# Optimization experiments

Hardware: AMD Instinct MI355X
Metric: run time of the kernel (lower is better)

Reference implementation:

```python
import jax, jax.numpy as jnp
import numpy as np

T, H, W = 4, 16, 16
S = T * H * W          # 1024 flattened sequence length
C = 576                # embd_dim
NH = 8                 # n_head
DK = C // NH           # 72 per-head dim
L = 4                  # n_layer
B = 4                  # batch
PD = C // 3            # 192 per-axis pos-embed dim


def setup_inputs() -> dict:
    key = jax.random.key(0)
    ks = jax.random.split(key, 10)
    s = 1.0 / np.sqrt(C)
    return {
        "x": jax.random.normal(ks[0], (B, T, H, W, C), jnp.float32),
        "pos0": jax.random.normal(ks[1], (T, PD), jnp.float32) * 0.01,
        "pos1": jax.random.normal(ks[2], (H, PD), jnp.float32) * 0.01,
        "pos2": jax.random.normal(ks[3], (W, PD), jnp.float32) * 0.01,
        "ln1_g": jnp.ones((L, C), jnp.float32),
        "ln1_b": jnp.zeros((L, C), jnp.float32),
        "wq": jax.random.normal(ks[4], (L, C, C), jnp.float32) * s,
        "wk": jax.random.normal(ks[5], (L, C, C), jnp.float32) * s,
        "wv": jax.random.normal(ks[6], (L, C, C), jnp.float32) * s,
        "wo": jax.random.normal(ks[7], (L, C, C), jnp.float32) * (s / np.sqrt(L)),
        "wo_b": jnp.zeros((L, C), jnp.float32),
        "ln2_g": jnp.ones((L, C), jnp.float32),
        "ln2_b": jnp.zeros((L, C), jnp.float32),
        "w1": jax.random.normal(ks[8], (L, C, 4 * C), jnp.float32) * s,
        "b1": jnp.zeros((L, 4 * C), jnp.float32),
        "w2": jax.random.normal(ks[9], (L, 4 * C, C), jnp.float32) * (s / 2.0),
        "b2": jnp.zeros((L, C), jnp.float32),
    }


def _layernorm(x, g, b):
    # Faithful to the source: float32 math, and (1e-5 + rsqrt(var)) multiplier
    # (note: source adds eps to rsqrt, not to var -- replicated exactly).
    xf = x.astype(jnp.float32)
    mu = xf.mean(-1, keepdims=True)
    var = jnp.mean(jnp.square(xf - mu), -1, keepdims=True)
    y = (xf - mu) * (1e-5 + jax.lax.rsqrt(var)) * g + b
    return y.astype(x.dtype)


def _stack(x, pos0, pos1, pos2, ln1_g, ln1_b, wq, wk, wv, wo, wo_b,
           ln2_g, ln2_b, w1, b1, w2, b2):
    b = x.shape[0]
    xf = x.reshape(b, S, C)
    # right_shift (decode_step=None): shift flattened tokens right by one
    xf = jnp.pad(xf[:, :-1], ((0, 0), (1, 0), (0, 0)))
    # broadcast positional embedding, concat along channel
    pos = jnp.concatenate([
        jnp.broadcast_to(pos0[:, None, None, :], (T, H, W, PD)),
        jnp.broadcast_to(pos1[None, :, None, :], (T, H, W, PD)),
        jnp.broadcast_to(pos2[None, None, :, :], (T, H, W, PD)),
    ], axis=-1).reshape(S, C)
    xf = xf + pos

    causal = jnp.tril(jnp.ones((S, S), bool))
    scale = 1.0 / np.sqrt(DK)
    neg_inf = jnp.float32(-jnp.inf)

    for l in range(L):  # fixed small layer loop
        # --- causal full self-attention ---
        h = _layernorm(xf, ln1_g[l], ln1_b[l])
        q = (h @ wq[l]).reshape(b, S, NH, DK).transpose(0, 2, 1, 3)
        k = (h @ wk[l]).reshape(b, S, NH, DK).transpose(0, 2, 1, 3)
        v = (h @ wv[l]).reshape(b, S, NH, DK).transpose(0, 2, 1, 3)
        att = jnp.einsum('bhqd,bhkd->bhqk', q, k) * scale
        att = jnp.where(causal, att, neg_inf)
        att = jax.nn.softmax(att, axis=-1)
        a = jnp.einsum('bhqk,bhkd->bhqd', att, v)
        a = a.transpose(0, 2, 1, 3).reshape(b, S, C)
        xf = xf + a @ wo[l] + wo_b[l]
        # --- FFN with GeLU2: sigmoid(1.702*x)*x ---
        h = _layernorm(xf, ln2_g[l], ln2_b[l])
        h = h @ w1[l] + b1[l]
        h = jax.nn.sigmoid(1.702 * h) * h
        xf = xf + h @ w2[l] + b2[l]
    return xf.reshape(b, T, H, W, C)


def reference(x, pos0, pos1, pos2, ln1_g, ln1_b, wq, wk, wv, wo, wo_b,
              ln2_g, ln2_b, w1, b1, w2, b2):
    return _stack(x, pos0, pos1, pos2, ln1_g, ln1_b, wq, wk, wv, wo, wo_b,
                  ln2_g, ln2_b, w1, b1, w2, b2)
```

## Files before the change

### kernel.cpp

```cpp
#include <hip/hip_runtime.h>
#include <hip/hip_bf16.h>

typedef __hip_bfloat16 bf16;
using bf16x8 = __attribute__((ext_vector_type(8))) short;
using f32x4  = __attribute__((ext_vector_type(4))) float;

#define S_LEN 1024
#define CDIM  576
#define NHEAD 8
#define DKH   72
#define BATCH 4
#define MROWS 4096
#define FFDIM 2304
#define QKVN  1728

__device__ __forceinline__ void gload16(const void* g, void* l) {
  __builtin_amdgcn_global_load_lds(
      (const __attribute__((address_space(1))) unsigned int*)g,
      (__attribute__((address_space(3))) unsigned int*)l, 16, 0, 0);
}

template <int N> __device__ __forceinline__ void wait_vmcnt() {
  if constexpr (N == 0)      asm volatile("s_waitcnt vmcnt(0)" ::: "memory");
  else if constexpr (N == 2) asm volatile("s_waitcnt vmcnt(2)" ::: "memory");
  else if constexpr (N == 3) asm volatile("s_waitcnt vmcnt(3)" ::: "memory");
  else if constexpr (N == 4) asm volatile("s_waitcnt vmcnt(4)" ::: "memory");
  else if constexpr (N == 6) asm volatile("s_waitcnt vmcnt(6)" ::: "memory");
}

__device__ __forceinline__ short f2bf_bits(float x) {
  unsigned int u = __float_as_uint(x);
  u += 0x7fffu + ((u >> 16) & 1u);
  return (short)(u >> 16);
}

__device__ __forceinline__ void transpose_body(
    float (*tile)[33], const float* in, bf16* out, int K, int N,
    size_t in_ls, size_t out_ls, int bx, int by, int z) {
  const float* inl = in + (size_t)z * in_ls;
  bf16* outl = out + (size_t)z * out_ls;
  int n0 = bx * 32, k0 = by * 32;
  int tx = threadIdx.x & 31, ty = threadIdx.x >> 5;
#pragma unroll
  for (int i = 0; i < 32; i += 8)
    tile[ty + i][tx] = inl[(size_t)(k0 + ty + i) * N + (n0 + tx)];
  __syncthreads();
#pragma unroll
  for (int i = 0; i < 32; i += 8)
    outl[(size_t)(n0 + ty + i) * K + (k0 + tx)] = __float2bfloat16(tile[tx][ty + i]);
}

__global__ __launch_bounds__(256) void prologue(
    const float* __restrict__ wq, const float* __restrict__ wk,
    const float* __restrict__ wv, const float* __restrict__ wo,
    const float* __restrict__ w1, const float* __restrict__ w2,
    bf16* __restrict__ wqkvT, bf16* __restrict__ woT,
    bf16* __restrict__ w1T, bf16* __restrict__ w2T,
    const float* __restrict__ x, const float* __restrict__ p0,
    const float* __restrict__ p1, const float* __restrict__ p2,
    float* __restrict__ xf) {
  __shared__ float tile[32][33];
  const size_t ils  = (size_t)CDIM * CDIM;
  const size_t ils2 = (size_t)CDIM * FFDIM;
  const size_t qkv_ls = (size_t)QKVN * CDIM;
  int r = blockIdx.x;
  if (r < 5184) {
    int which = r / 1296, rr = r % 1296;
    int z = rr / 324, rem = rr % 324;
    int bx = rem % 18, by = rem / 18;
    const float* in; bf16* out; size_t ols;
    if (which == 0)      { in = wq; out = wqkvT;                       ols = qkv_ls; }
    else if (which == 1) { in = wk; out = wqkvT + (size_t)CDIM * CDIM; ols = qkv_ls; }
    else if (which == 2) { in = wv; out = wqkvT + (size_t)2 * CDIM * CDIM; ols = qkv_ls; }
    else                 { in = wo; out = woT;                         ols = ils; }
    transpose_body(tile, in, out, CDIM, CDIM, ils, ols, bx, by, z);
  } else if (r < 10368) {
    int rr = r - 5184;
    int z = rr / 1296, rem = rr % 1296;
    int bx = rem % 72, by = rem / 72;
    transpose_body(tile, w1, w1T, CDIM, FFDIM, ils2, ils2, bx, by, z);
  } else if (r < 15552) {
    int rr = r - 10368;
    int z = rr / 1296, rem = rr % 1296;
    int bx = rem % 18, by = rem / 18;
    transpose_body(tile, w2, w2T, FFDIM, CDIM, ils2, ils2, bx, by, z);
  } else {
    int idx = (r - 15552) * 256 + threadIdx.x;
    int c4 = idx % 144;
    int s  = (idx / 144) & (S_LEN - 1);
    int b  = idx / (144 * S_LEN);
    int c  = c4 * 4;
    int t = s >> 8, hh = (s >> 4) & 15, w = s & 15;
    float4 pv;
    if (c < 192)       pv = *(const float4*)&p0[t  * 192 + c];
    else if (c < 384)  pv = *(const float4*)&p1[hh * 192 + c - 192];
    else               pv = *(const float4*)&p2[w  * 192 + c - 384];
    float4 xv = make_float4(0.f, 0.f, 0.f, 0.f);
    if (s > 0) xv = *(const float4*)&x[((size_t)b * S_LEN + s - 1) * CDIM + c];
    float4 rr4 = make_float4(xv.x + pv.x, xv.y + pv.y, xv.z + pv.z, xv.w + pv.w);
    *(float4*)&xf[((size_t)b * S_LEN + s) * CDIM + c] = rr4;
  }
}

__global__ __launch_bounds__(256) void ln_kernel(
    const float* __restrict__ x, const float* __restrict__ g,
    const float* __restrict__ b, bf16* __restrict__ out) {
  int row  = blockIdx.x * 4 + (threadIdx.x >> 6);
  int lane = threadIdx.x & 63;
  const float* xr = x + (size_t)row * CDIM;
  float vals[9];
  float sum = 0.f;
#pragma unroll
  for (int i = 0; i < 9; i++) { vals[i] = xr[lane + 64 * i]; sum += vals[i]; }
#pragma unroll
  for (int o = 1; o < 64; o <<= 1) sum += __shfl_xor(sum, o);
  float mu = sum * (1.f / CDIM);
  float vs = 0.f;
#pragma unroll
  for (int i = 0; i < 9; i++) { float d = vals[i] - mu; vs += d * d; }
#pragma unroll
  for (int o = 1; o < 64; o <<= 1) vs += __shfl_xor(vs, o);
  float mult = 1e-5f + rsqrtf(vs * (1.f / CDIM));
  bf16* orow = out + (size_t)row * CDIM;
#pragma unroll
  for (int i = 0; i < 9; i++) {
    int c = lane + 64 * i;
    orow[c] = __float2bfloat16((vals[i] - mu) * mult * g[c] + b[c]);
  }
}

template <int BM, int BN, bool BIAS, bool RES, int ACT, bool OUTBF>
__global__ __launch_bounds__(256) void gemm3(
    const bf16* __restrict__ A, const bf16* __restrict__ Bt,
    const float* __restrict__ bias, const float* __restrict__ res,
    void* __restrict__ outp, int N, int K) {
  constexpr int MI = BM / 32;
  constexpr int NI = BN / 32;
  constexpr int AJ = BM / 64;
  constexpr int BJ = BN / 64;
  constexpr int LPS = AJ + BJ;
  __shared__ __align__(16) short ldsA[4][BM * 32];
  __shared__ __align__(16) short ldsB[4][BN * 32];
  const int tid = threadIdx.x, lane = tid & 63, wave = tid >> 6;
  const int lr = lane & 15, quad = lane >> 4;
  const int m0 = blockIdx.x * BM, n0 = blockIdx.y * BN;
  const int wm = (wave & 1) * (BM / 2), wn = (wave >> 1) * (BN / 2);
  f32x4 acc[MI][NI] = {};

  const int srow = lane >> 2, scol = (lane & 3) * 8;
  const short* Ag[AJ];
  int ldsAo[AJ];
#pragma unroll
  for (int j = 0; j < AJ; j++) {
    Ag[j] = (const short*)A + (size_t)(m0 + (wave * AJ + j) * 16 + srow) * K + scol;
    ldsAo[j] = (wave * AJ + j) * 512;
  }
  const short* Bg[BJ];
  int ldsBo[BJ];
#pragma unroll
  for (int j = 0; j < BJ; j++) {
    Bg[j] = (const short*)Bt + (size_t)(n0 + (wave * BJ + j) * 16 + srow) * K + scol;
    ldsBo[j] = (wave * BJ + j) * 512;
  }

#pragma unroll
  for (int j = 0; j < AJ; j++) gload16(Ag[j], &ldsA[0][ldsAo[j]]);
#pragma unroll
  for (int j = 0; j < BJ; j++) gload16(Bg[j], &ldsB[0][ldsBo[j]]);
#pragma unroll
  for (int j = 0; j < AJ; j++) gload16(Ag[j] + 32, &ldsA[1][ldsAo[j]]);
#pragma unroll
  for (int j = 0; j < BJ; j++) gload16(Bg[j] + 32, &ldsB[1][ldsBo[j]]);

  int bi = 0;
  for (int k0 = 0; k0 < K; k0 += 32, bi = (bi + 1) & 3) {
    if (k0 + 64 < K) {
      const int sb = (bi + 2) & 3;
#pragma unroll
      for (int j = 0; j < AJ; j++) gload16(Ag[j] + k0 + 64, &ldsA[sb][ldsAo[j]]);
#pragma unroll
      for (int j = 0; j < BJ; j++) gload16(Bg[j] + k0 + 64, &ldsB[sb][ldsBo[j]]);
      wait_vmcnt<2 * LPS>();
    } else if (k0 + 32 < K) {
      wait_vmcnt<LPS>();
    } else {
      wait_vmcnt<0>();
    }
    __builtin_amdgcn_s_barrier();
    __builtin_amdgcn_sched_barrier(0);
    bf16x8 af[MI], bfv[NI];
#pragma unroll
    for (int mi = 0; mi < MI; mi++)
      af[mi] = *(const bf16x8*)&ldsA[bi][(wm + mi * 16 + lr) * 32 + quad * 8];
#pragma unroll
    for (int ni = 0; ni < NI; ni++)
      bfv[ni] = *(const bf16x8*)&ldsB[bi][(wn + ni * 16 + lr) * 32 + quad * 8];
#pragma unroll
    for (int mi = 0; mi < MI; mi++)
#pragma unroll
      for (int ni = 0; ni < NI; ni++)
        acc[mi][ni] = __builtin_amdgcn_mfma_f32_16x16x32_bf16(af[mi], bfv[ni], acc[mi][ni], 0, 0, 0);
  }

  float* fout = (float*)outp;
  bf16*  bout = (bf16*)outp;
#pragma unroll
  for (int mi = 0; mi < MI; mi++)
#pragma unroll
    for (int ni = 0; ni < NI; ni++) {
      int col = n0 + wn + ni * 16 + lr;
#pragma unroll
      for (int r = 0; r < 4; r++) {
        int row = m0 + wm + mi * 16 + quad * 4 + r;
        float v = acc[mi][ni][r];
        if (BIAS) v += bias[col];
        if (ACT == 1) v = v / (1.f + __expf(-1.702f * v));
        size_t idx = (size_t)row * N + col;
        if (RES) v += res[idx];
        if (OUTBF) bout[idx] = __float2bfloat16(v);
        else       fout[idx] = v;
      }
    }
}

__global__ __launch_bounds__(256) void attn_mfma(
    const bf16* __restrict__ qkv, bf16* __restrict__ a) {
  __shared__ __align__(16) short ldsK[2][9 * 512];
  __shared__ __align__(16) short ldsVt[2][80][104];
  __shared__ __align__(16) short ldsP[4 * 1024];
  const int bh = blockIdx.y, b = bh >> 3, h = bh & 7;
  const int tid = threadIdx.x, wave = tid >> 6, lane = tid & 63;
  const int lr = lane & 15, quad = lane >> 4;
  const int qt = (blockIdx.y < 16) ? (15 - (int)blockIdx.x) : (int)blockIdx.x;
  const float scale = 0.11785113019775793f;
  const int qcol = h * DKH, kcol = CDIM + h * DKH, vcol = 2 * CDIM + h * DKH;

  const int qrow = qt * 64 + wave * 16 + lr;
  const short* qg = (const short*)qkv + (size_t)(b * S_LEN + qrow) * QKVN + qcol;
  bf16x8 qfrag[3];
#pragma unroll
  for (int c = 0; c < 3; c++) {
    int d0 = c * 32 + quad * 8;
    bf16x8 z = {0, 0, 0, 0, 0, 0, 0, 0};
    qfrag[c] = (d0 < DKH) ? *(const bf16x8*)(qg + d0) : z;
  }
  f32x4 oacc[5] = {};
  float m[4], l[4];
#pragma unroll
  for (int r = 0; r < 4; r++) { m[r] = -1e30f; l[r] = 0.f; }

  const size_t ktstep = (size_t)64 * QKVN;
  const short* kg0 = (const short*)qkv + (size_t)(b * S_LEN + wave * 16 + lr) * QKVN + kcol + quad * 8;
  const short* kg2 = (const short*)qkv + (size_t)(b * S_LEN + lane) * QKVN + kcol + 64;
  const int vkey = tid & 63, vdgb = tid >> 6;
  const short* vg0 = (const short*)qkv + (size_t)(b * S_LEN + vkey) * QKVN + vcol;

  {
#pragma unroll
    for (int c = 0; c < 2; c++)
      gload16(kg0 + c * 32, &ldsK[0][(wave * 2 + c) * 512]);
    if (wave == 0) gload16(kg2, &ldsK[0][8 * 512]);
#pragma unroll
    for (int pass = 0; pass < 3; pass++) {
      int d0 = (vdgb + pass * 4) * 8;
      if (d0 < 80) {
        bf16x8 vv = {0, 0, 0, 0, 0, 0, 0, 0};
        if (d0 < DKH) vv = *(const bf16x8*)(vg0 + d0);
#pragma unroll
        for (int j = 0; j < 8; j++) ldsVt[0][d0 + j][vkey] = vv[j];
      }
    }
  }
  __syncthreads();

  for (int kt = 0; kt <= qt; kt++) {
    const int cur = kt & 1, nxt = cur ^ 1;
    const bool pf = (kt < qt);
    bf16x8 vpre[3];
    if (pf) {
      const short* kg = kg0 + (size_t)(kt + 1) * ktstep;
#pragma unroll
      for (int c = 0; c < 2; c++)
        gload16(kg + c * 32, &ldsK[nxt][(wave * 2 + c) * 512]);
      if (wave == 0) gload16(kg2 + (size_t)(kt + 1) * ktstep, &ldsK[nxt][8 * 512]);
      const short* vg = vg0 + (size_t)(kt + 1) * ktstep;
#pragma unroll
      for (int pass = 0; pass < 3; pass++) {
        int d0 = (vdgb + pass * 4) * 8;
        bf16x8 z = {0, 0, 0, 0, 0, 0, 0, 0};
        vpre[pass] = (d0 < DKH) ? *(const bf16x8*)(vg + d0) : z;
      }
    }
    f32x4 sacc[4] = {};
    __builtin_amdgcn_s_setprio(1);
#pragma unroll
    for (int nc = 0; nc < 4; nc++) {
      bf16x8 kf0 = *(const bf16x8*)&ldsK[cur][(nc * 2 + 0) * 512 + lane * 8];
      sacc[nc] = __builtin_amdgcn_mfma_f32_16x16x32_bf16(qfrag[0], kf0, sacc[nc], 0, 0, 0);
      bf16x8 kf1 = *(const bf16x8*)&ldsK[cur][(nc * 2 + 1) * 512 + lane * 8];
      sacc[nc] = __builtin_amdgcn_mfma_f32_16x16x32_bf16(qfrag[1], kf1, sacc[nc], 0, 0, 0);
      bf16x8 kf2 = *(const bf16x8*)&ldsK[cur][8 * 512 + (nc * 16 + lr) * 8];
      sacc[nc] = __builtin_amdgcn_mfma_f32_16x16x32_bf16(qfrag[2], kf2, sacc[nc], 0, 0, 0);
    }
    __builtin_amdgcn_s_setprio(0);
    float pmax[4];
#pragma unroll
    for (int r = 0; r < 4; r++) pmax[r] = -1e30f;
    bool diag = (kt == qt);
#pragma unroll
    for (int nc = 0; nc < 4; nc++)
#pragma unroll
      for (int r = 0; r < 4; r++) {
        float s = sacc[nc][r] * scale;
        if (diag && (nc * 16 + lr > wave * 16 + quad * 4 + r)) s = -1e30f;
        sacc[nc][r] = s;
        pmax[r] = fmaxf(pmax[r], s);
      }
    bool within = (pmax[0] - m[0] <= 8.f) && (pmax[1] - m[1] <= 8.f) &&
                  (pmax[2] - m[2] <= 8.f) && (pmax[3] - m[3] <= 8.f);
    if (!__all(within)) {
      float tmax[4];
#pragma unroll
      for (int r = 0; r < 4; r++) {
        tmax[r] = pmax[r];
        tmax[r] = fmaxf(tmax[r], __shfl_xor(tmax[r], 1));
        tmax[r] = fmaxf(tmax[r], __shfl_xor(tmax[r], 2));
        tmax[r] = fmaxf(tmax[r], __shfl_xor(tmax[r], 4));
        tmax[r] = fmaxf(tmax[r], __shfl_xor(tmax[r], 8));
      }
#pragma unroll
      for (int r = 0; r < 4; r++) {
        float mn = fmaxf(m[r], tmax[r]);
        float alpha = __expf(m[r] - mn);
        m[r] = mn;
        l[r] *= alpha;
#pragma unroll
        for (int dc = 0; dc < 5; dc++) oacc[dc][r] *= alpha;
      }
    }
    float psum[4];
#pragma unroll
    for (int r = 0; r < 4; r++) psum[r] = 0.f;
#pragma unroll
    for (int nc = 0; nc < 4; nc++)
#pragma unroll
      for (int r = 0; r < 4; r++) {
        float p = __expf(sacc[nc][r] - m[r]);
        psum[r] += p;
        int col = nc * 16 + lr;
        ldsP[wave * 1024 + (col >> 5) * 512 +
             (((col >> 3) & 3) * 16 + quad * 4 + r) * 8 + (col & 7)] = f2bf_bits(p);
      }
    bf16x8 pfrag[2];
#pragma unroll
    for (int kc = 0; kc < 2; kc++)
      pfrag[kc] = *(const bf16x8*)&ldsP[wave * 1024 + kc * 512 + lane * 8];
    __builtin_amdgcn_s_setprio(1);
#pragma unroll
    for (int dc = 0; dc < 5; dc++)
#pragma unroll
      for (int kc = 0; kc < 2; kc++) {
        bf16x8 vf = *(const bf16x8*)&ldsVt[cur][dc * 16 + lr][kc * 32 + quad * 8];
        oacc[dc] = __builtin_amdgcn_mfma_f32_16x16x32_bf16(pfrag[kc], vf, oacc[dc], 0, 0, 0);
      }
    __builtin_amdgcn_s_setprio(0);
#pragma unroll
    for (int r = 0; r < 4; r++) {
      psum[r] += __shfl_xor(psum[r], 1);
      psum[r] += __shfl_xor(psum[r], 2);
      psum[r] += __shfl_xor(psum[r], 4);
      psum[r] += __shfl_xor(psum[r], 8);
      l[r] += psum[r];
    }
    if (pf) {
#pragma unroll
      for (int pass = 0; pass < 3; pass++) {
        int d0 = (vdgb + pass * 4) * 8;
        if (d0 < 80) {
#pragma unroll
          for (int j = 0; j < 8; j++) ldsVt[nxt][d0 + j][vkey] = vpre[pass][j];
        }
      }
    }
    __syncthreads();
  }

#pragma unroll
  for (int dc = 0; dc < 5; dc++) {
    int d = dc * 16 + lr;
    if (d < DKH) {
#pragma unroll
      for (int r = 0; r < 4; r++) {
        int row = qt * 64 + wave * 16 + quad * 4 + r;
        float val = oacc[dc][r] / l[r];
        a[(size_t)(b * S_LEN + row) * CDIM + h * DKH + d] = __float2bfloat16(val);
      }
    }
  }
}

extern "C" void kernel_launch(void* const* d_in, const int* in_sizes, int n_in,
                              void* d_out, int out_size, void* d_ws, size_t ws_size,
                              hipStream_t stream) {
  const float* x    = (const float*)d_in[0];
  const float* pos0 = (const float*)d_in[1];
  const float* pos1 = (const float*)d_in[2];
  const float* pos2 = (const float*)d_in[3];
  const float* ln1g = (const float*)d_in[4];
  const float* ln1b = (const float*)d_in[5];
  const float* wq   = (const float*)d_in[6];
  const float* wk   = (const float*)d_in[7];
  const float* wv   = (const float*)d_in[8];
  const float* wo   = (const float*)d_in[9];
  const float* wob  = (const float*)d_in[10];
  const float* ln2g = (const float*)d_in[11];
  const float* ln2b = (const float*)d_in[12];
  const float* w1   = (const float*)d_in[13];
  const float* b1   = (const float*)d_in[14];
  const float* w2   = (const float*)d_in[15];
  const float* b2   = (const float*)d_in[16];

  char* ws = (char*)d_ws;
  size_t off = 0;
  auto alloc = [&](size_t bytes) {
    char* p = ws + off;
    off += (bytes + 255) & ~(size_t)255;
    return p;
  };
  bf16* wqkvT = (bf16*)alloc((size_t)4 * QKVN * CDIM * sizeof(bf16));
  bf16* woT   = (bf16*)alloc((size_t)4 * CDIM * CDIM * sizeof(bf16));
  bf16* w1T   = (bf16*)alloc((size_t)4 * FFDIM * CDIM * sizeof(bf16));
  bf16* w2T   = (bf16*)alloc((size_t)4 * CDIM * FFDIM * sizeof(bf16));
  bf16* hbuf  = (bf16*)alloc((size_t)MROWS * CDIM * sizeof(bf16));
  bf16* abuf  = (bf16*)alloc((size_t)MROWS * CDIM * sizeof(bf16));
  bf16* ubuf  = (bf16*)alloc((size_t)MROWS * FFDIM * sizeof(bf16));
  bf16* qkvb  = (bf16*)alloc((size_t)MROWS * QKVN * sizeof(bf16));
  float* xf   = (float*)d_out;

  const size_t ils  = (size_t)CDIM * CDIM;
  const size_t ils2 = (size_t)CDIM * FFDIM;
  const size_t qkv_ls = (size_t)QKVN * CDIM;

  prologue<<<17856, 256, 0, stream>>>(wq, wk, wv, wo, w1, w2,
                                      wqkvT, woT, w1T, w2T,
                                      x, pos0, pos1, pos2, xf);

  for (int l = 0; l < 4; l++) {
    bf16* wqkv_l = wqkvT + (size_t)l * qkv_ls;
    bf16* wo_l   = woT   + (size_t)l * ils;
    bf16* w1_l   = w1T   + (size_t)l * ils2;
    bf16* w2_l   = w2T   + (size_t)l * ils2;

    ln_kernel<<<1024, 256, 0, stream>>>(xf, ln1g + l * CDIM, ln1b + l * CDIM, hbuf);
    gemm3<128, 64, false, false, 0, true><<<dim3(32, QKVN / 64), 256, 0, stream>>>(
        hbuf, wqkv_l, nullptr, nullptr, qkvb, QKVN, CDIM);
    attn_mfma<<<dim3(16, 32), 256, 0, stream>>>(qkvb, abuf);
    gemm3<64, 64, true, true, 0, false><<<dim3(64, CDIM / 64), 256, 0, stream>>>(
        abuf, wo_l, wob + l * CDIM, xf, xf, CDIM, CDIM);
    ln_kernel<<<1024, 256, 0, stream>>>(xf, ln2g + l * CDIM, ln2b + l * CDIM, hbuf);
    gemm3<128, 64, true, false, 1, true><<<dim3(32, FFDIM / 64), 256, 0, stream>>>(
        hbuf, w1_l, b1 + l * FFDIM, nullptr, ubuf, FFDIM, CDIM);
    gemm3<64, 64, true, true, 0, false><<<dim3(64, CDIM / 64), 256, 0, stream>>>(
        ubuf, w2_l, b2 + l * CDIM, xf, xf, CDIM, FFDIM);
  }
}
```

Baseline: 671.5 us.

## Fuse LayerNorm into residual GEMM epilogue via last-block row-panel counter

The residual-adding GEMMs (attention output projection and FFN down projection) now perform the following LayerNorm themselves. Each block increments an atomic counter for its 64-row panel, and the last block to finish normalizes those rows into the bf16 buffer. This removes seven separate ln_kernel launches and their extra pass over xf. In exchange it adds thread fences and atomics, and the LayerNorm for each panel is serialized onto a single block at the tail of the GEMM. Counters are zeroed in the prologue and each layer uses its own counter slice.

```diff
diff --git a/kernel.cpp b/kernel.cpp
--- a/kernel.cpp
+++ b/kernel.cpp
@@ -58,7 +58,7 @@
     bf16* __restrict__ w1T, bf16* __restrict__ w2T,
     const float* __restrict__ x, const float* __restrict__ p0,
     const float* __restrict__ p1, const float* __restrict__ p2,
-    float* __restrict__ xf) {
+    float* __restrict__ xf, int* __restrict__ ctr) {
   __shared__ float tile[32][33];
   const size_t ils  = (size_t)CDIM * CDIM;
   const size_t ils2 = (size_t)CDIM * FFDIM;
@@ -85,6 +85,10 @@
     int bx = rem % 18, by = rem / 18;
     transpose_body(tile, w2, w2T, FFDIM, CDIM, ils2, ils2, bx, by, z);
   } else {
+    if (r == 15552) {
+      ctr[threadIdx.x] = 0;
+      ctr[threadIdx.x + 256] = 0;
+    }
     int idx = (r - 15552) * 256 + threadIdx.x;
     int c4 = idx % 144;
     int s  = (idx / 144) & (S_LEN - 1);
@@ -129,11 +133,13 @@
   }
 }
 
-template <int BM, int BN, bool BIAS, bool RES, int ACT, bool OUTBF>
+template <int BM, int BN, bool BIAS, bool RES, int ACT, bool OUTBF, bool LNF>
 __global__ __launch_bounds__(256) void gemm3(
     const bf16* __restrict__ A, const bf16* __restrict__ Bt,
     const float* __restrict__ bias, const float* __restrict__ res,
-    void* __restrict__ outp, int N, int K) {
+    void* __restrict__ outp, int N, int K,
+    const float* __restrict__ lng, const float* __restrict__ lnb,
+    bf16* __restrict__ lnout, int* __restrict__ ctr) {
   constexpr int MI = BM / 32;
   constexpr int NI = BN / 32;
   constexpr int AJ = BM / 64;
@@ -221,6 +227,42 @@
         else       fout[idx] = v;
       }
     }
+
+  if (LNF) {
+    __threadfence();
+    __syncthreads();
+    __shared__ int sfin;
+    if (tid == 0) sfin = atomicAdd(&ctr[blockIdx.x], 1);
+    __syncthreads();
+    if (sfin == (int)gridDim.y - 1) {
+      __threadfence();
+      const int lnlane = tid & 63;
+#pragma unroll 1
+      for (int it = 0; it < 16; ++it) {
+        int row = m0 + it * 4 + (tid >> 6);
+        const float* xr = fout + (size_t)row * CDIM;
+        float vals[9];
+        float sum = 0.f;
+#pragma unroll
+        for (int i = 0; i < 9; i++) { vals[i] = xr[lnlane + 64 * i]; sum += vals[i]; }
+#pragma unroll
+        for (int o = 1; o < 64; o <<= 1) sum += __shfl_xor(sum, o);
+        float mu = sum * (1.f / CDIM);
+        float vs = 0.f;
+#pragma unroll
+        for (int i = 0; i < 9; i++) { float d = vals[i] - mu; vs += d * d; }
+#pragma unroll
+        for (int o = 1; o < 64; o <<= 1) vs += __shfl_xor(vs, o);
+        float mult = 1e-5f + rsqrtf(vs * (1.f / CDIM));
+        bf16* orow = lnout + (size_t)row * CDIM;
+#pragma unroll
+        for (int i = 0; i < 9; i++) {
+          int c = lnlane + 64 * i;
+          orow[c] = __float2bfloat16((vals[i] - mu) * mult * lng[c] + lnb[c]);
+        }
+      }
+    }
+  }
 }
 
 __global__ __launch_bounds__(256) void attn_mfma(
@@ -435,6 +477,7 @@
   bf16* abuf  = (bf16*)alloc((size_t)MROWS * CDIM * sizeof(bf16));
   bf16* ubuf  = (bf16*)alloc((size_t)MROWS * FFDIM * sizeof(bf16));
   bf16* qkvb  = (bf16*)alloc((size_t)MROWS * QKVN * sizeof(bf16));
+  int*  ctrs  = (int*)alloc(512 * sizeof(int));
   float* xf   = (float*)d_out;
 
   const size_t ils  = (size_t)CDIM * CDIM;
@@ -443,7 +486,8 @@
 
   prologue<<<17856, 256, 0, stream>>>(wq, wk, wv, wo, w1, w2,
                                       wqkvT, woT, w1T, w2T,
-                                      x, pos0, pos1, pos2, xf);
+                                      x, pos0, pos1, pos2, xf, ctrs);
+  ln_kernel<<<1024, 256, 0, stream>>>(xf, ln1g, ln1b, hbuf);
 
   for (int l = 0; l < 4; l++) {
     bf16* wqkv_l = wqkvT + (size_t)l * qkv_ls;
@@ -451,16 +495,24 @@
     bf16* w1_l   = w1T   + (size_t)l * ils2;
     bf16* w2_l   = w2T   + (size_t)l * ils2;
 
-    ln_kernel<<<1024, 256, 0, stream>>>(xf, ln1g + l * CDIM, ln1b + l * CDIM, hbuf);
-    gemm3<128, 64, false, false, 0, true><<<dim3(32, QKVN / 64), 256, 0, stream>>>(
-        hbuf, wqkv_l, nullptr, nullptr, qkvb, QKVN, CDIM);
+    gemm3<128, 64, false, false, 0, true, false><<<dim3(32, QKVN / 64), 256, 0, stream>>>(
+        hbuf, wqkv_l, nullptr, nullptr, qkvb, QKVN, CDIM,
+        nullptr, nullptr, nullptr, nullptr);
     attn_mfma<<<dim3(16, 32), 256, 0, stream>>>(qkvb, abuf);
-    gemm3<64, 64, true, true, 0, false><<<dim3(64, CDIM / 64), 256, 0, stream>>>(
-        abuf, wo_l, wob + l * CDIM, xf, xf, CDIM, CDIM);
-    ln_kernel<<<1024, 256, 0, stream>>>(xf, ln2g + l * CDIM, ln2b + l * CDIM, hbuf);
-    gemm3<128, 64, true, false, 1, true><<<dim3(32, FFDIM / 64), 256, 0, stream>>>(
-        hbuf, w1_l, b1 + l * FFDIM, nullptr, ubuf, FFDIM, CDIM);
-    gemm3<64, 64, true, true, 0, false><<<dim3(64, CDIM / 64), 256, 0, stream>>>(
-        ubuf, w2_l, b2 + l * CDIM, xf, xf, CDIM, FFDIM);
-  }
-}
+    gemm3<64, 64, true, true, 0, false, true><<<dim3(64, CDIM / 64), 256, 0, stream>>>(
+        abuf, wo_l, wob + l * CDIM, xf, xf, CDIM, CDIM,
+        ln2g + l * CDIM, ln2b + l * CDIM, hbuf, ctrs + l * 64);
+    gemm3<128, 64, true, false, 1, true, false><<<dim3(32, FFDIM / 64), 256, 0, stream>>>(
+        hbuf, w1_l, b1 + l * FFDIM, nullptr, ubuf, FFDIM, CDIM,
+        nullptr, nullptr, nullptr, nullptr);
+    if (l < 3) {
+      gemm3<64, 64, true, true, 0, false, true><<<dim3(64, CDIM / 64), 256, 0, stream>>>(
+          ubuf, w2_l, b2 + l * CDIM, xf, xf, CDIM, FFDIM,
+          ln1g + (l + 1) * CDIM, ln1b + (l + 1) * CDIM, hbuf, ctrs + 256 + l * 64);
+    } else {
+      gemm3<64, 64, true, true, 0, false, false><<<dim3(64, CDIM / 64), 256, 0, stream>>>(
+          ubuf, w2_l, b2 + l * CDIM, xf, xf, CDIM, FFDIM,
+          nullptr, nullptr, nullptr, nullptr);
+    }
+  }
+}
```

Measured after the change: 1.220 ms. 81.6% more time.
